# Optimization experiments

Measured on AMD Instinct MI355X. Metric: run time of the kernel, lower is better.

Reference implementation:

```python
import jax, jax.numpy as jnp
import numpy as np

D_MODEL = 1024
NUM_HEADS = 16
D_K = D_MODEL // NUM_HEADS
B, S = 4, 2048
NEG_INF = -1e9


def _linear_params(key, d_out, d_in):
    k1, k2 = jax.random.split(key)
    lim = 1.0 / np.sqrt(d_in)
    w = jax.random.uniform(k1, (d_out, d_in), jnp.float32, -lim, lim)
    b = jax.random.uniform(k2, (d_out,), jnp.float32, -lim, lim)
    return w, b


def setup_inputs() -> dict:
    key = jax.random.key(0)
    ks = jax.random.split(key, 16)
    query = jax.random.normal(ks[0], (B, S, D_MODEL), jnp.float32)
    kk = jax.random.normal(ks[1], (B, S, D_MODEL), jnp.float32)
    vv = jax.random.normal(ks[2], (B, S, D_MODEL), jnp.float32)
    # causal mask, broadcastable to [B,H,Sq,Sk]
    mask = jnp.tril(jnp.ones((S, S), jnp.int32))[None, None]
    wq1, bq1 = _linear_params(ks[3], D_MODEL, D_MODEL)
    wq2, bq2 = _linear_params(ks[4], D_MODEL, D_MODEL)
    wk1, bk1 = _linear_params(ks[5], D_MODEL, D_MODEL)
    wk2, bk2 = _linear_params(ks[6], D_MODEL, D_MODEL)
    wv1, bv1 = _linear_params(ks[7], D_MODEL, D_MODEL)
    wv2, bv2 = _linear_params(ks[8], D_MODEL, D_MODEL)
    wo, bo = _linear_params(ks[9], D_MODEL, D_MODEL)
    return dict(query=query, key=kk, value=vv, mask=mask,
                wq1=wq1, bq1=bq1, wq2=wq2, bq2=bq2,
                wk1=wk1, bk1=bk1, wk2=wk2, bk2=bk2,
                wv1=wv1, bv1=bv1, wv2=wv2, bv2=bv2,
                wo=wo, bo=bo)


def _swiglu_proj(x, w1, b1, w2, b2):
    # F.silu(w1(x)) * w2(x)
    return jax.nn.silu(x @ w1.T + b1) * (x @ w2.T + b2)


def _split_heads(x):
    b, s, _ = x.shape
    return x.reshape(b, s, NUM_HEADS, D_K).transpose(0, 2, 1, 3)  # [B,H,S,dk]


def reference(query, key, value, mask,
              wq1, bq1, wq2, bq2,
              wk1, bk1, wk2, bk2,
              wv1, bv1, wv2, bv2,
              wo, bo):
    q = _split_heads(_swiglu_proj(query, wq1, bq1, wq2, bq2))
    k = _split_heads(_swiglu_proj(key, wk1, bk1, wk2, bk2))
    v = _split_heads(_swiglu_proj(value, wv1, bv1, wv2, bv2))
    scores = jnp.einsum('bhqd,bhkd->bhqk', q, k) / np.sqrt(D_K).astype(np.float32)
    scores = jnp.where(mask == 0, jnp.float32(NEG_INF), scores)
    attn = jax.nn.softmax(scores, axis=-1)
    x = jnp.einsum('bhqk,bhkd->bhqd', attn, v)  # [B,H,S,dk]
    x = x.transpose(0, 2, 1, 3).reshape(query.shape[0], -1, NUM_HEADS * D_K)
    return x @ wo.T + bo
```

## Files before the change

kernel.cpp:

```cpp
#include <hip/hip_runtime.h>


typedef __bf16 bf16;
typedef bf16 bf16x8 __attribute__((ext_vector_type(8)));
typedef float f32x4 __attribute__((ext_vector_type(4)));
typedef unsigned short u16;
typedef unsigned int u32;
typedef u16 u16x8 __attribute__((ext_vector_type(8)));
typedef u16 u16x4 __attribute__((ext_vector_type(4)));

#define DEVI static __device__ __forceinline__

DEVI u16 f2b(float f) {
  union { float f; u32 u; } v; v.f = f;
  u32 r = v.u + 0x7FFFu + ((v.u >> 16) & 1u);
  return (u16)(r >> 16);
}
DEVI f32x4 mfma16(bf16x8 a, bf16x8 b, f32x4 c) {
  return __builtin_amdgcn_mfma_f32_16x16x32_bf16(a, b, c, 0, 0, 0);
}
DEVI void gload16(const void* g, void* l) {
  __builtin_amdgcn_global_load_lds(
      (const __attribute__((address_space(1))) void*)g,
      (__attribute__((address_space(3))) void*)l, 16, 0, 0);
}
DEVI u32 cvtpk(float lo, float hi) {
  u32 r;
  asm("v_cvt_pk_bf16_f32 %0, %1, %2" : "=v"(r) : "v"(lo), "v"(hi));
  return r;
}
DEVI void pswap(u32& a, u32& b) {
  asm("v_permlane32_swap_b32 %0, %1" : "+v"(a), "+v"(b));
}

struct P6 { const float* p[6]; };

__global__ void cvt_wpair(P6 in, u16* __restrict__ out) {
  const int pair = blockIdx.y;
  const float* w1 = in.p[2 * pair];
  const float* w2 = in.p[2 * pair + 1];
  u16* dst = out + (size_t)pair * 2097152;
  const int i = blockIdx.x * 256 + threadIdx.x;
  const int v = i >> 7;
  const int k0 = (i & 127) << 3;
  const int t7 = v & 127;
  const int g = (t7 >> 4) & 1;
  const int c = (v >> 7) * 64 + ((t7 >> 5) << 4) + (t7 & 15);
  const float* src = (g ? w2 : w1) + (size_t)c * 1024 + k0;
  const f32x4 a = *(const f32x4*)src;
  const f32x4 b = *(const f32x4*)(src + 4);
  u16x8 wv;
#pragma unroll
  for (int j = 0; j < 4; ++j) { wv[j] = f2b(a[j]); wv[4 + j] = f2b(b[j]); }
  *(u16x8*)(dst + (size_t)v * 1024 + k0) = wv;
}

__global__ void cvt_x(const float* __restrict__ s0, u16* __restrict__ d0,
                      const float* __restrict__ s1, u16* __restrict__ d1) {
  const float* src = blockIdx.y ? s1 : s0;
  u16* dst = blockIdx.y ? d1 : d0;
  const int i = blockIdx.x * 256 + threadIdx.x;
  const f32x4 a = ((const f32x4*)src)[i * 2];
  const f32x4 b = ((const f32x4*)src)[i * 2 + 1];
  u16x8 w;
#pragma unroll
  for (int j = 0; j < 4; ++j) { w[j] = f2b(a[j]); w[4 + j] = f2b(b[j]); }
  ((u16x8*)dst)[i] = w;
}

struct GArgs {
  const u16* A; const u16* W;
  const float* b1; const float* b2;
  void* out; float scale;
};

template<int MODE, bool DUAL>
__global__ __launch_bounds__(512, 2) void gemm256(GArgs g0, GArgs g1)
{
  extern __shared__ char smem[];
  const int fl = blockIdx.x;
  const GArgs g = (DUAL && fl >= 512) ? g1 : g0;
  const int local = DUAL ? (fl & 511) : fl;
  const int t = threadIdx.x;
  const int lane = t & 63, wid = t >> 6;
  const int lg = lane >> 4, lc = lane & 15;
  const int wr = (wid >> 1) * 64;
  const int wc = (wid & 1) * 64;
  constexpr int NXB = (MODE == 2) ? 8 : 16;
  const int xcd = local & 7, w8 = local >> 3;
  const int m0 = (xcd * 4 + w8 / NXB) * 256;
  const int bx = w8 % NXB;
  const int K = 1024;
  const int srow = lane >> 3, scolb = (lane & 7) << 4;

  const f32x4 fz = {0.f, 0.f, 0.f, 0.f};
  f32x4 acc[4][4];
#pragma unroll
  for (int i = 0; i < 4; ++i)
#pragma unroll
    for (int j = 0; j < 4; ++j) acc[i][j] = fz;

  auto STAGE = [&](int buf, int kt) {
    const int k0 = kt << 6;
    char* As = smem + buf * 49152;
    char* Ws = As + 32768;
#pragma unroll
    for (int p = 0; p < 4; ++p) {
      const int rb = wid * 32 + p * 8;
      const int row = rb + srow;
      const int ce = (scolb ^ ((row & 7) << 4)) >> 1;
      gload16(g.A + (size_t)(m0 + row) * K + k0 + ce, As + rb * 128);
    }
#pragma unroll
    for (int p = 0; p < 2; ++p) {
      const int rb = wid * 16 + p * 8;
      const int row = rb + srow;
      const int ce = (scolb ^ ((row & 7) << 4)) >> 1;
      gload16(g.W + (size_t)(bx * 128 + row) * K + k0 + ce, Ws + rb * 128);
    }
  };

  STAGE(0, 0);
  __syncthreads();
  for (int kt = 0; kt < 16; ++kt) {
    const int cur = kt & 1;
    if (kt < 15) STAGE(cur ^ 1, kt + 1);
    const char* As = smem + cur * 49152;
    const char* Ws = As + 32768;
#pragma unroll
    for (int kh = 0; kh < 2; ++kh) {
      bf16x8 af[4], bfr[4];
#pragma unroll
      for (int mf = 0; mf < 4; ++mf) {
        const int r = wr + mf * 16 + lc;
        af[mf] = *(const bf16x8*)(As + r * 128 + ((kh * 64 + (lg << 4)) ^ ((r & 7) << 4)));
      }
#pragma unroll
      for (int nf = 0; nf < 4; ++nf) {
        const int v = wc + nf * 16 + lc;
        bfr[nf] = *(const bf16x8*)(Ws + v * 128 + ((kh * 64 + (lg << 4)) ^ ((v & 7) << 4)));
      }
#pragma unroll
      for (int mf = 0; mf < 4; ++mf)
#pragma unroll
        for (int nf = 0; nf < 4; ++nf)
          acc[mf][nf] = mfma16(af[mf], bfr[nf], acc[mf][nf]);
    }
    __syncthreads();
  }
  if constexpr (MODE == 2) {
    float* Co = (float*)g.out;
#pragma unroll
    for (int mf = 0; mf < 4; ++mf)
#pragma unroll
      for (int nf = 0; nf < 4; ++nf) {
        const int r0 = m0 + wr + mf * 16 + (lg << 2);
        const int C = bx * 128 + wc + nf * 16 + lc;
        const float bv = g.b1[C];
#pragma unroll
        for (int j = 0; j < 4; ++j)
          Co[(size_t)(r0 + j) * 1024 + C] = acc[mf][nf][j] + bv;
      }
  } else {
    u16* Co = (u16*)g.out;
#pragma unroll
    for (int mf = 0; mf < 4; ++mf) {
      const int r0 = m0 + wr + mf * 16 + (lg << 2);
#pragma unroll
      for (int p = 0; p < 2; ++p) {
        const int C = bx * 64 + (wid & 1) * 32 + p * 16 + lc;
        const float b1v = g.b1[C], b2v = g.b2[C];
        const int h = C >> 6, d = C & 63;
        if constexpr (MODE == 0) {
#pragma unroll
          for (int j = 0; j < 4; ++j) {
            const int r = r0 + j;
            const float x = acc[mf][2 * p][j] + b1v;
            const float y = acc[mf][2 * p + 1][j] + b2v;
            const float vv = (x / (1.f + __expf(-x))) * y * g.scale;
            const int bb = r >> 11, s = r & 2047;
            Co[((size_t)(bb * 16 + h) * 2048 + s) * 64 + d] = f2b(vv);
          }
        } else {
          u16x4 wv;
#pragma unroll
          for (int j = 0; j < 4; ++j) {
            const float x = acc[mf][2 * p][j] + b1v;
            const float y = acc[mf][2 * p + 1][j] + b2v;
            wv[j] = f2b((x / (1.f + __expf(-x))) * y);
          }
          const int bb = r0 >> 11, s0 = r0 & 2047;
          *(u16x4*)(Co + ((size_t)(bb * 16 + h) * 64 + d) * 2048 + s0) = wv;
        }
      }
    }
  }
}

__global__ __launch_bounds__(256, 4) void attn_fwd(
    const u16* __restrict__ Q, const u16* __restrict__ Kk,
    const u16* __restrict__ Vt, u16* __restrict__ O)
{
  __shared__ char smem[32768];
  const int t = threadIdx.x;
  const int lane = t & 63, wid = t >> 6;
  const int lg = lane >> 4, lc = lane & 15;
  const int flat = blockIdx.y * 16 + blockIdx.x;
  const int fl2 = (flat & 7) * 128 + (flat >> 3);
  const int qi = fl2 & 15;
  const int bh = fl2 >> 4;
  const int b = bh >> 4, h = bh & 15;
  const f32x4 fz = {0.f, 0.f, 0.f, 0.f};
  const float THR = 11.5f;
  const bool ev = ((lg & 1) == 0);

  auto STAGE = [&](int buf, int kt) {
    const int kbase = kt << 6;
    char* Kb = smem + buf * 16384;
    char* Vb = Kb + 8192;
#pragma unroll
    for (int p = 0; p < 4; ++p) {
      const int idx = wid * 4 + p;
      const int rb = (idx & 7) * 8;
      const int row = rb + (lane >> 3);
      const int ce = (((lane & 7) << 4) ^ ((row & 7) << 4)) >> 1;
      if (idx < 8)
        gload16(Kk + ((size_t)bh * 2048 + kbase + row) * 64 + ce, Kb + rb * 128);
      else
        gload16(Vt + ((size_t)bh * 64 + row) * 2048 + kbase + ce, Vb + rb * 128);
    }
  };

  for (int pass = 0; pass < 2; ++pass) {
    const int qc = pass ? (31 - qi) : qi;
    const int qw = qc * 64 + wid * 16;

    bf16x8 qf[2];
#pragma unroll
    for (int kh = 0; kh < 2; ++kh)
      qf[kh] = *(const bf16x8*)(Q + ((size_t)bh * 2048 + qw + lc) * 64 + kh * 32 + lg * 8);

    f32x4 o[4];
#pragma unroll
    for (int dn = 0; dn < 4; ++dn) o[dn] = fz;
    float mrow = -1e30f, lsum = 0.f;

    const int nt = qc + 1;
    STAGE(0, 0);
    __syncthreads();
    for (int kt = 0; kt < nt; ++kt) {
      const int cur = kt & 1;
      if (kt + 1 < nt) STAGE(cur ^ 1, kt + 1);
      const char* Ks = smem + cur * 16384;
      const char* Vs = Ks + 8192;
      f32x4 sfT[4];
#pragma unroll
      for (int nf = 0; nf < 4; ++nf) sfT[nf] = fz;
      __builtin_amdgcn_s_setprio(1);
#pragma unroll
      for (int kh = 0; kh < 2; ++kh) {
        bf16x8 kb[4];
#pragma unroll
        for (int nf = 0; nf < 4; ++nf) {
          const int r = nf * 16 + lc;
          kb[nf] = *(const bf16x8*)(Ks + r * 128 + ((kh * 64 + (lg << 4)) ^ ((r & 7) << 4)));
        }
#pragma unroll
        for (int nf = 0; nf < 4; ++nf)
          sfT[nf] = mfma16(kb[nf], qf[kh], sfT[nf]);
      }
      __builtin_amdgcn_s_setprio(0);
      if (kt == nt - 1) {
        const int kb0 = kt * 64 + (lg << 2);
        const int qq = qw + lc;
#pragma unroll
        for (int nf = 0; nf < 4; ++nf)
#pragma unroll
          for (int j = 0; j < 4; ++j)
            if (kb0 + nf * 16 + j > qq) sfT[nf][j] = -1e30f;
      }
      float pm = sfT[0][0];
#pragma unroll
      for (int nf = 0; nf < 4; ++nf)
#pragma unroll
        for (int j = 0; j < 4; ++j) pm = fmaxf(pm, sfT[nf][j]);
      pm = fmaxf(pm, __shfl_xor(pm, 16));
      pm = fmaxf(pm, __shfl_xor(pm, 32));
      if (!__all(pm <= mrow + THR)) {
        const float mn = fmaxf(mrow, pm);
        const float sc = exp2f(mrow - mn);
        mrow = mn;
        lsum *= sc;
#pragma unroll
        for (int dn = 0; dn < 4; ++dn)
#pragma unroll
          for (int j = 0; j < 4; ++j) o[dn][j] *= sc;
      }
      float p[4][4];
#pragma unroll
      for (int nf = 0; nf < 4; ++nf)
#pragma unroll
        for (int j = 0; j < 4; ++j) {
          p[nf][j] = exp2f(sfT[nf][j] - mrow);
          lsum += p[nf][j];
        }
      u32 pw[2][4];
#pragma unroll
      for (int kh = 0; kh < 2; ++kh) {
        u32 A0 = cvtpk(p[2 * kh][0], p[2 * kh][1]);
        u32 A1 = cvtpk(p[2 * kh][2], p[2 * kh][3]);
        u32 B0 = cvtpk(p[2 * kh + 1][0], p[2 * kh + 1][1]);
        u32 B1 = cvtpk(p[2 * kh + 1][2], p[2 * kh + 1][3]);
        pswap(A0, B0);
        pswap(A1, B1);
        const u32 P0s = __shfl_xor(A0, 16);
        const u32 Q0s = __shfl_xor(B0, 16);
        const u32 P1s = __shfl_xor(A1, 16);
        const u32 Q1s = __shfl_xor(B1, 16);
        pw[kh][0] = ev ? A0 : Q0s;
        pw[kh][1] = ev ? A1 : Q1s;
        pw[kh][2] = ev ? P0s : B0;
        pw[kh][3] = ev ? P1s : B1;
      }
      __builtin_amdgcn_s_setprio(1);
#pragma unroll
      for (int kh = 0; kh < 2; ++kh) {
        union { u32 u[4]; bf16x8 v; } pc;
#pragma unroll
        for (int w = 0; w < 4; ++w) pc.u[w] = pw[kh][w];
        const bf16x8 pa = pc.v;
#pragma unroll
        for (int dn = 0; dn < 4; ++dn) {
          const int vr = dn * 16 + lc;
          const bf16x8 vb = *(const bf16x8*)(Vs + vr * 128 + ((kh * 64 + (lg << 4)) ^ ((vr & 7) << 4)));
          o[dn] = mfma16(vb, pa, o[dn]);
        }
      }
      __builtin_amdgcn_s_setprio(0);
      __syncthreads();
    }
    lsum += __shfl_xor(lsum, 16);
    lsum += __shfl_xor(lsum, 32);
    const float inv = __builtin_amdgcn_rcpf(lsum);
    const size_t ob = ((size_t)(b * 2048 + qw + lc) * 16 + h) * 64 + (lg << 2);
#pragma unroll
    for (int dn = 0; dn < 4; ++dn) {
      u16x4 wv;
#pragma unroll
      for (int j = 0; j < 4; ++j) wv[j] = f2b(o[dn][j] * inv);
      *(u16x4*)(O + ob + dn * 16) = wv;
    }
  }
}

extern "C" void kernel_launch(void* const* d_in, const int* in_sizes, int n_in,
                              void* d_out, int out_size, void* d_ws, size_t ws_size,
                              hipStream_t stream)
{
  (void)in_sizes; (void)n_in; (void)out_size; (void)ws_size;
  const float* xq  = (const float*)d_in[0];
  const float* xk  = (const float*)d_in[1];
  const float* xv  = (const float*)d_in[2];
  const float* wq1 = (const float*)d_in[4];
  const float* bq1 = (const float*)d_in[5];
  const float* wq2 = (const float*)d_in[6];
  const float* bq2 = (const float*)d_in[7];
  const float* wk1 = (const float*)d_in[8];
  const float* bk1 = (const float*)d_in[9];
  const float* wk2 = (const float*)d_in[10];
  const float* bk2 = (const float*)d_in[11];
  const float* wv1 = (const float*)d_in[12];
  const float* bv1 = (const float*)d_in[13];
  const float* wv2 = (const float*)d_in[14];
  const float* bv2 = (const float*)d_in[15];
  const float* wo  = (const float*)d_in[16];
  const float* bo  = (const float*)d_in[17];

  char* ws = (char*)d_ws;
  u16* WB = (u16*)ws;
  u16* XQ = (u16*)(ws + 14680064);
  u16* XK = (u16*)(ws + 31457280);
  u16* QB = (u16*)(ws + 48234496);
  u16* KB = (u16*)(ws + 65011712);
  u16* VT = (u16*)(ws + 81788928);
  u16* XV = XQ;
  u16* AO = XK;
  u16* WCQ = WB;
  u16* WCK = WB + 2097152;
  u16* WCV = WB + 4194304;
  u16* WO  = WB + 6291456;

  P6 p6 = {{wq1, wq2, wk1, wk2, wv1, wv2}};
  cvt_wpair<<<dim3(1024, 3), 256, 0, stream>>>(p6, WB);
  cvt_x<<<dim3(512, 1), 256, 0, stream>>>(wo, WO, wo, WO);
  cvt_x<<<dim3(4096, 2), 256, 0, stream>>>(xq, XQ, xk, XK);

  const float QSCALE = 0.125f * 1.44269504088896f;
  GArgs gq = {XQ, WCQ, bq1, bq2, QB, QSCALE};
  GArgs gk = {XK, WCK, bk1, bk2, KB, 1.0f};
  gemm256<0, true><<<1024, 512, 98304, stream>>>(gq, gk);

  cvt_x<<<dim3(4096, 1), 256, 0, stream>>>(xv, XV, xv, XV);
  GArgs gv = {XV, WCV, bv1, bv2, VT, 1.0f};
  gemm256<1, false><<<512, 512, 98304, stream>>>(gv, gv);

  attn_fwd<<<dim3(16, 64), 256, 0, stream>>>(QB, KB, VT, AO);

  GArgs go = {AO, WO, bo, nullptr, d_out, 1.0f};
  gemm256<2, false><<<256, 512, 98304, stream>>>(go, go);
}
```

Baseline: 244.6 us.

## Rewrite attention as single-wave blocks loading K/V directly into registers

The attention kernel moves from 256-thread blocks that staged K/V tiles in shared memory with double buffering and barriers to 64-thread single-wave blocks. Each block handles 32 query rows as two 16-row groups and loads K and V tiles straight from global memory into registers, with K prefetched one tile ahead. This removes LDS traffic and __syncthreads, and reuses each K/V register fragment across two query groups. In exchange, K/V reuse across waves in a block is lost, so global/L2 traffic rises, register pressure grows, and the causal triangle is tiled at 32-row granularity against 64-key tiles.

```diff
diff --git a/kernel.cpp b/kernel.cpp
--- a/kernel.cpp
+++ b/kernel.cpp
@@ -197,158 +197,178 @@
   }
 }
 
-__global__ __launch_bounds__(256, 4) void attn_fwd(
+__global__ __launch_bounds__(64, 2) void attn_fwd(
     const u16* __restrict__ Q, const u16* __restrict__ Kk,
     const u16* __restrict__ Vt, u16* __restrict__ O)
 {
-  __shared__ char smem[32768];
-  const int t = threadIdx.x;
-  const int lane = t & 63, wid = t >> 6;
+  const int lane = threadIdx.x;
   const int lg = lane >> 4, lc = lane & 15;
-  const int flat = blockIdx.y * 16 + blockIdx.x;
-  const int fl2 = (flat & 7) * 128 + (flat >> 3);
-  const int qi = fl2 & 15;
-  const int bh = fl2 >> 4;
+  const int flat = blockIdx.y * 32 + blockIdx.x;
+  const int fl2 = (flat & 7) * 256 + (flat >> 3);
+  const int qi = fl2 & 31;
+  const int bh = fl2 >> 5;
   const int b = bh >> 4, h = bh & 15;
   const f32x4 fz = {0.f, 0.f, 0.f, 0.f};
   const float THR = 11.5f;
   const bool ev = ((lg & 1) == 0);
 
-  auto STAGE = [&](int buf, int kt) {
-    const int kbase = kt << 6;
-    char* Kb = smem + buf * 16384;
-    char* Vb = Kb + 8192;
-#pragma unroll
-    for (int p = 0; p < 4; ++p) {
-      const int idx = wid * 4 + p;
-      const int rb = (idx & 7) * 8;
-      const int row = rb + (lane >> 3);
-      const int ce = (((lane & 7) << 4) ^ ((row & 7) << 4)) >> 1;
-      if (idx < 8)
-        gload16(Kk + ((size_t)bh * 2048 + kbase + row) * 64 + ce, Kb + rb * 128);
-      else
-        gload16(Vt + ((size_t)bh * 64 + row) * 2048 + kbase + ce, Vb + rb * 128);
-    }
-  };
+  const u16* Kb = Kk + (size_t)bh * 2048 * 64;
+  const u16* Vb = Vt + (size_t)bh * 64 * 2048;
 
   for (int pass = 0; pass < 2; ++pass) {
-    const int qc = pass ? (31 - qi) : qi;
-    const int qw = qc * 64 + wid * 16;
-
-    bf16x8 qf[2];
-#pragma unroll
-    for (int kh = 0; kh < 2; ++kh)
-      qf[kh] = *(const bf16x8*)(Q + ((size_t)bh * 2048 + qw + lc) * 64 + kh * 32 + lg * 8);
-
-    f32x4 o[4];
-#pragma unroll
-    for (int dn = 0; dn < 4; ++dn) o[dn] = fz;
-    float mrow = -1e30f, lsum = 0.f;
-
-    const int nt = qc + 1;
-    STAGE(0, 0);
-    __syncthreads();
-    for (int kt = 0; kt < nt; ++kt) {
-      const int cur = kt & 1;
-      if (kt + 1 < nt) STAGE(cur ^ 1, kt + 1);
-      const char* Ks = smem + cur * 16384;
-      const char* Vs = Ks + 8192;
-      f32x4 sfT[4];
-#pragma unroll
-      for (int nf = 0; nf < 4; ++nf) sfT[nf] = fz;
+    const int qc = pass ? (63 - qi) : qi;
+    const int qw = qc * 32;
+    const int nt = (qc >> 1) + 1;
+
+    bf16x8 qf[2][2];
+#pragma unroll
+    for (int qg = 0; qg < 2; ++qg)
+#pragma unroll
+      for (int kh = 0; kh < 2; ++kh)
+        qf[qg][kh] = *(const bf16x8*)(Q + ((size_t)bh * 2048 + qw + qg * 16 + lc) * 64 + kh * 32 + lg * 8);
+
+    f32x4 o[2][4];
+#pragma unroll
+    for (int qg = 0; qg < 2; ++qg)
+#pragma unroll
+      for (int dn = 0; dn < 4; ++dn) o[qg][dn] = fz;
+    float mrow[2] = {-1e30f, -1e30f}, lsum[2] = {0.f, 0.f};
+
+    bf16x8 kra[8], krb[8], vr[8];
+
+    auto LOADK = [&](bf16x8 (&kr)[8], int kt) {
+      const int kbase = kt << 6;
+#pragma unroll
+      for (int nf = 0; nf < 4; ++nf)
+#pragma unroll
+        for (int kh = 0; kh < 2; ++kh)
+          kr[nf * 2 + kh] = *(const bf16x8*)(Kb + (size_t)(kbase + nf * 16 + lc) * 64 + kh * 32 + lg * 8);
+    };
+
+    auto BODY = [&](bf16x8 (&kr)[8], int kt) {
+      const int kbase = kt << 6;
+#pragma unroll
+      for (int dn = 0; dn < 4; ++dn)
+#pragma unroll
+        for (int kh = 0; kh < 2; ++kh)
+          vr[dn * 2 + kh] = *(const bf16x8*)(Vb + (size_t)(dn * 16 + lc) * 2048 + kbase + kh * 32 + lg * 8);
+      f32x4 sfT[4][2];
+#pragma unroll
+      for (int nf = 0; nf < 4; ++nf)
+#pragma unroll
+        for (int qg = 0; qg < 2; ++qg) sfT[nf][qg] = fz;
       __builtin_amdgcn_s_setprio(1);
 #pragma unroll
-      for (int kh = 0; kh < 2; ++kh) {
-        bf16x8 kb[4];
+      for (int kh = 0; kh < 2; ++kh)
 #pragma unroll
         for (int nf = 0; nf < 4; ++nf) {
-          const int r = nf * 16 + lc;
-          kb[nf] = *(const bf16x8*)(Ks + r * 128 + ((kh * 64 + (lg << 4)) ^ ((r & 7) << 4)));
-        }
-#pragma unroll
-        for (int nf = 0; nf < 4; ++nf)
-          sfT[nf] = mfma16(kb[nf], qf[kh], sfT[nf]);
-      }
+          sfT[nf][0] = mfma16(kr[nf * 2 + kh], qf[0][kh], sfT[nf][0]);
+          sfT[nf][1] = mfma16(kr[nf * 2 + kh], qf[1][kh], sfT[nf][1]);
+        }
       __builtin_amdgcn_s_setprio(0);
       if (kt == nt - 1) {
-        const int kb0 = kt * 64 + (lg << 2);
-        const int qq = qw + lc;
+#pragma unroll
+        for (int qg = 0; qg < 2; ++qg) {
+          const int qq = qw + qg * 16 + lc;
+#pragma unroll
+          for (int nf = 0; nf < 4; ++nf)
+#pragma unroll
+            for (int j = 0; j < 4; ++j)
+              if (kbase + nf * 16 + (lg << 2) + j > qq) sfT[nf][qg][j] = -1e30f;
+        }
+      }
+      float pm[2];
+#pragma unroll
+      for (int qg = 0; qg < 2; ++qg) {
+        float m = sfT[0][qg][0];
 #pragma unroll
         for (int nf = 0; nf < 4; ++nf)
 #pragma unroll
-          for (int j = 0; j < 4; ++j)
-            if (kb0 + nf * 16 + j > qq) sfT[nf][j] = -1e30f;
-      }
-      float pm = sfT[0][0];
-#pragma unroll
-      for (int nf = 0; nf < 4; ++nf)
-#pragma unroll
-        for (int j = 0; j < 4; ++j) pm = fmaxf(pm, sfT[nf][j]);
-      pm = fmaxf(pm, __shfl_xor(pm, 16));
-      pm = fmaxf(pm, __shfl_xor(pm, 32));
-      if (!__all(pm <= mrow + THR)) {
-        const float mn = fmaxf(mrow, pm);
-        const float sc = exp2f(mrow - mn);
-        mrow = mn;
-        lsum *= sc;
-#pragma unroll
-        for (int dn = 0; dn < 4; ++dn)
-#pragma unroll
-          for (int j = 0; j < 4; ++j) o[dn][j] *= sc;
-      }
-      float p[4][4];
-#pragma unroll
-      for (int nf = 0; nf < 4; ++nf)
-#pragma unroll
-        for (int j = 0; j < 4; ++j) {
-          p[nf][j] = exp2f(sfT[nf][j] - mrow);
-          lsum += p[nf][j];
-        }
-      u32 pw[2][4];
+          for (int j = 0; j < 4; ++j) m = fmaxf(m, sfT[nf][qg][j]);
+        m = fmaxf(m, __shfl_xor(m, 16));
+        m = fmaxf(m, __shfl_xor(m, 32));
+        pm[qg] = m;
+      }
+      const bool ok = (pm[0] <= mrow[0] + THR) && (pm[1] <= mrow[1] + THR);
+      if (!__all(ok)) {
+#pragma unroll
+        for (int qg = 0; qg < 2; ++qg) {
+          const float mn = fmaxf(mrow[qg], pm[qg]);
+          const float sc = exp2f(mrow[qg] - mn);
+          mrow[qg] = mn;
+          lsum[qg] *= sc;
+#pragma unroll
+          for (int dn = 0; dn < 4; ++dn)
+#pragma unroll
+            for (int j = 0; j < 4; ++j) o[qg][dn][j] *= sc;
+        }
+      }
+#pragma unroll
+      for (int qg = 0; qg < 2; ++qg)
+#pragma unroll
+        for (int nf = 0; nf < 4; ++nf)
+#pragma unroll
+          for (int j = 0; j < 4; ++j) {
+            const float p = exp2f(sfT[nf][qg][j] - mrow[qg]);
+            sfT[nf][qg][j] = p;
+            lsum[qg] += p;
+          }
+      u32 pw[2][2][4];
+#pragma unroll
+      for (int qg = 0; qg < 2; ++qg)
+#pragma unroll
+        for (int kh = 0; kh < 2; ++kh) {
+          u32 A0 = cvtpk(sfT[2 * kh][qg][0], sfT[2 * kh][qg][1]);
+          u32 A1 = cvtpk(sfT[2 * kh][qg][2], sfT[2 * kh][qg][3]);
+          u32 B0 = cvtpk(sfT[2 * kh + 1][qg][0], sfT[2 * kh + 1][qg][1]);
+          u32 B1 = cvtpk(sfT[2 * kh + 1][qg][2], sfT[2 * kh + 1][qg][3]);
+          pswap(A0, B0);
+          pswap(A1, B1);
+          const u32 P0s = __shfl_xor(A0, 16);
+          const u32 Q0s = __shfl_xor(B0, 16);
+          const u32 P1s = __shfl_xor(A1, 16);
+          const u32 Q1s = __shfl_xor(B1, 16);
+          pw[qg][kh][0] = ev ? A0 : Q0s;
+          pw[qg][kh][1] = ev ? A1 : Q1s;
+          pw[qg][kh][2] = ev ? P0s : B0;
+          pw[qg][kh][3] = ev ? P1s : B1;
+        }
+      __builtin_amdgcn_s_setprio(1);
 #pragma unroll
       for (int kh = 0; kh < 2; ++kh) {
-        u32 A0 = cvtpk(p[2 * kh][0], p[2 * kh][1]);
-        u32 A1 = cvtpk(p[2 * kh][2], p[2 * kh][3]);
-        u32 B0 = cvtpk(p[2 * kh + 1][0], p[2 * kh + 1][1]);
-        u32 B1 = cvtpk(p[2 * kh + 1][2], p[2 * kh + 1][3]);
-        pswap(A0, B0);
-        pswap(A1, B1);
-        const u32 P0s = __shfl_xor(A0, 16);
-        const u32 Q0s = __shfl_xor(B0, 16);
-        const u32 P1s = __shfl_xor(A1, 16);
-        const u32 Q1s = __shfl_xor(B1, 16);
-        pw[kh][0] = ev ? A0 : Q0s;
-        pw[kh][1] = ev ? A1 : Q1s;
-        pw[kh][2] = ev ? P0s : B0;
-        pw[kh][3] = ev ? P1s : B1;
-      }
-      __builtin_amdgcn_s_setprio(1);
-#pragma unroll
-      for (int kh = 0; kh < 2; ++kh) {
-        union { u32 u[4]; bf16x8 v; } pc;
-#pragma unroll
-        for (int w = 0; w < 4; ++w) pc.u[w] = pw[kh][w];
-        const bf16x8 pa = pc.v;
+        union { u32 u[4]; bf16x8 v; } p0, p1;
+#pragma unroll
+        for (int w = 0; w < 4; ++w) { p0.u[w] = pw[0][kh][w]; p1.u[w] = pw[1][kh][w]; }
 #pragma unroll
         for (int dn = 0; dn < 4; ++dn) {
-          const int vr = dn * 16 + lc;
-          const bf16x8 vb = *(const bf16x8*)(Vs + vr * 128 + ((kh * 64 + (lg << 4)) ^ ((vr & 7) << 4)));
-          o[dn] = mfma16(vb, pa, o[dn]);
+          o[0][dn] = mfma16(vr[dn * 2 + kh], p0.v, o[0][dn]);
+          o[1][dn] = mfma16(vr[dn * 2 + kh], p1.v, o[1][dn]);
         }
       }
       __builtin_amdgcn_s_setprio(0);
-      __syncthreads();
-    }
-    lsum += __shfl_xor(lsum, 16);
-    lsum += __shfl_xor(lsum, 32);
-    const float inv = __builtin_amdgcn_rcpf(lsum);
-    const size_t ob = ((size_t)(b * 2048 + qw + lc) * 16 + h) * 64 + (lg << 2);
-#pragma unroll
-    for (int dn = 0; dn < 4; ++dn) {
-      u16x4 wv;
-#pragma unroll
-      for (int j = 0; j < 4; ++j) wv[j] = f2b(o[dn][j] * inv);
-      *(u16x4*)(O + ob + dn * 16) = wv;
+    };
+
+    LOADK(kra, 0);
+    for (int kt = 0; kt < nt; kt += 2) {
+      if (kt + 1 < nt) LOADK(krb, kt + 1);
+      BODY(kra, kt);
+      if (kt + 2 < nt) LOADK(kra, kt + 2);
+      if (kt + 1 < nt) BODY(krb, kt + 1);
+    }
+#pragma unroll
+    for (int qg = 0; qg < 2; ++qg) {
+      float l = lsum[qg];
+      l += __shfl_xor(l, 16);
+      l += __shfl_xor(l, 32);
+      const float inv = __builtin_amdgcn_rcpf(l);
+      const size_t ob = ((size_t)(b * 2048 + qw + qg * 16 + lc) * 16 + h) * 64 + (lg << 2);
+#pragma unroll
+      for (int dn = 0; dn < 4; ++dn) {
+        u16x4 wv;
+#pragma unroll
+        for (int j = 0; j < 4; ++j) wv[j] = f2b(o[qg][dn][j] * inv);
+        *(u16x4*)(O + ob + dn * 16) = wv;
+      }
     }
   }
 }
@@ -404,7 +424,7 @@
   GArgs gv = {XV, WCV, bv1, bv2, VT, 1.0f};
   gemm256<1, false><<<512, 512, 98304, stream>>>(gv, gv);
 
-  attn_fwd<<<dim3(16, 64), 256, 0, stream>>>(QB, KB, VT, AO);
+  attn_fwd<<<dim3(32, 64), 64, 0, stream>>>(QB, KB, VT, AO);
 
   GArgs go = {AO, WO, bo, nullptr, d_out, 1.0f};
   gemm256<2, false><<<256, 512, 98304, stream>>>(go, go);
```

Measured after the change: 290.4 us. 1.19x slower.
